# Kernel optimization log

Measured on AMD Instinct MI355X. Metric: run time of the kernel, lower is better.

Reference implementation:

```python
import jax, jax.numpy as jnp
import numpy as np

L, B, S, H = 4, 2, 2048, 1024
NH, HD, FFN = 16, 64, 4096
EPS = 1e-5


def setup_inputs() -> dict:
    key = jax.random.key(0)
    ks = jax.random.split(key, 6)
    std = 0.02
    return {
        "hidden_states": jax.random.normal(ks[0], (B, S, H), jnp.float32),
        "ln1_g": jnp.ones((L, H), jnp.float32),
        "ln1_b": jnp.zeros((L, H), jnp.float32),
        "Wqkv": jax.random.normal(ks[1], (L, H, 3 * H), jnp.float32) * std,
        "Wproj": jax.random.normal(ks[2], (L, H, H), jnp.float32) * std,
        "ln2_g": jnp.ones((L, H), jnp.float32),
        "ln2_b": jnp.zeros((L, H), jnp.float32),
        "Wfc1": jax.random.normal(ks[3], (L, H, FFN), jnp.float32) * std,
        "Wfc2": jax.random.normal(ks[4], (L, FFN, H), jnp.float32) * std,
        "lnf_g": jnp.ones((H,), jnp.float32),
        "lnf_b": jnp.zeros((H,), jnp.float32),
    }


def _layernorm(x, g, b):
    mu = jnp.mean(x, axis=-1, keepdims=True)
    var = jnp.mean(jnp.square(x - mu), axis=-1, keepdims=True)
    return (x - mu) * jax.lax.rsqrt(var + EPS) * g + b


def _block_forward(x, ln1_g, ln1_b, Wqkv, Wproj, ln2_g, ln2_b, Wfc1, Wfc2, lnf_g, lnf_b):
    scale = HD ** -0.5
    causal = jnp.tril(jnp.ones((S, S), bool))  # [S, S]

    def layer(x, p):
        g1, b1, wqkv, wproj, g2, b2, wfc1, wfc2 = p
        # Attention sub-block (pre-norm)
        h = _layernorm(x, g1, b1)
        qkv = (h @ wqkv).reshape(B, S, 3, NH, HD)
        q, k, v = qkv[:, :, 0], qkv[:, :, 1], qkv[:, :, 2]  # [B,S,NH,HD]
        scores = jnp.einsum("bqhd,bkhd->bhqk", q, k) * scale
        scores = jnp.where(causal, scores, -jnp.inf)
        probs = jax.nn.softmax(scores, axis=-1)
        attn = jnp.einsum("bhqk,bkhd->bqhd", probs, v).reshape(B, S, H)
        x = x + attn @ wproj
        # FFN sub-block (pre-norm)
        h = _layernorm(x, g2, b2)
        h = jax.nn.gelu(h @ wfc1, approximate=False) @ wfc2
        return x + h, None

    x, _ = jax.lax.scan(layer, x, (ln1_g, ln1_b, Wqkv, Wproj, ln2_g, ln2_b, Wfc1, Wfc2))
    return _layernorm(x, lnf_g, lnf_b)


def reference(hidden_states, ln1_g, ln1_b, Wqkv, Wproj, ln2_g, ln2_b, Wfc1, Wfc2, lnf_g, lnf_b):
    return _block_forward(hidden_states, ln1_g, ln1_b, Wqkv, Wproj, ln2_g, ln2_b, Wfc1, Wfc2, lnf_g, lnf_b)
```

## Files before the change

### kernel.cpp

```cpp
#include <hip/hip_runtime.h>
#include <hip/hip_bf16.h>
#include <math.h>

#define LYRS 4
#define BB   2
#define SS   2048
#define HH   1024
#define NHD  16
#define HDD  64
#define FFN_ 4096
#define BS   (BB*SS)
#define EPS_ 1e-5f

typedef __attribute__((ext_vector_type(8))) __bf16 bf16x8;
typedef __attribute__((ext_vector_type(4))) __bf16 bf16x4;
typedef __attribute__((ext_vector_type(4))) float f32x4;
typedef __attribute__((address_space(1))) void* gas_t;
typedef __attribute__((address_space(3))) void* las_t;

__device__ inline void async16(void* lds, const void* g) {
    __builtin_amdgcn_global_load_lds((gas_t)g, (las_t)lds, 16, 0, 0);
}

__device__ inline void storev(float* p, float v) { *p = v; }
__device__ inline void storev(__hip_bfloat16* p, float v) { *p = __float2bfloat16(v); }

template <typename OutT>
__global__ void ln_k(const float* __restrict__ x, const float* __restrict__ g,
                     const float* __restrict__ b, OutT* __restrict__ y) {
    const int row = blockIdx.x;
    const int tid = threadIdx.x;
    const float* xr = x + (size_t)row * HH;

    float v[4];
    float s = 0.f, s2 = 0.f;
#pragma unroll
    for (int i = 0; i < 4; ++i) {
        v[i] = xr[tid + i * 256];
        s  += v[i];
        s2 += v[i] * v[i];
    }
#pragma unroll
    for (int o = 1; o < 64; o <<= 1) {
        s  += __shfl_xor(s,  o);
        s2 += __shfl_xor(s2, o);
    }
    __shared__ float sh[8];
    const int wave = tid >> 6, lane = tid & 63;
    if (lane == 0) { sh[wave] = s; sh[4 + wave] = s2; }
    __syncthreads();
    if (tid == 0) {
        float ts  = sh[0] + sh[1] + sh[2] + sh[3];
        float ts2 = sh[4] + sh[5] + sh[6] + sh[7];
        float mu  = ts * (1.f / HH);
        sh[0] = mu;
        sh[1] = ts2 * (1.f / HH) - mu * mu;
    }
    __syncthreads();
    const float mu   = sh[0];
    const float rstd = rsqrtf(sh[1] + EPS_);
#pragma unroll
    for (int i = 0; i < 4; ++i) {
        int c = tid + i * 256;
        storev(&y[(size_t)row * HH + c], (v[i] - mu) * rstd * g[c] + b[c]);
    }
}

__global__ __launch_bounds__(256) void transpose_cast(const float* __restrict__ W,
                                                      __hip_bfloat16* __restrict__ WT,
                                                      int K, int N) {
    __shared__ float t[32][33];
    const int n0 = blockIdx.x * 32, k0 = blockIdx.y * 32;
    const int tx = threadIdx.x & 31, ty8 = threadIdx.x >> 5;
#pragma unroll
    for (int i = 0; i < 4; ++i) {
        int k = ty8 + i * 8;
        t[k][tx] = W[(size_t)(k0 + k) * N + n0 + tx];
    }
    __syncthreads();
#pragma unroll
    for (int i = 0; i < 4; ++i) {
        int n = ty8 + i * 8;
        WT[(size_t)(n0 + n) * K + k0 + tx] = __float2bfloat16(t[tx][n]);
    }
}

template <bool GELU, bool RES, int SPLITK, typename OutT>
__global__ __launch_bounds__(256) void gemm_bf16(
    const __hip_bfloat16* __restrict__ A,
    const __hip_bfloat16* __restrict__ BT,
    const float* __restrict__ R,
    OutT* __restrict__ C,
    int M, int N, int K)
{
    __shared__ unsigned short As[2][128 * 32];
    __shared__ unsigned short Bs[2][128 * 32];

    const int tid  = threadIdx.x;
    const int lane = tid & 63;
    const int wv   = tid >> 6;
    const int wy   = wv >> 1, wx = wv & 1;
    const int nby  = M >> 7;
    const int tiles = nby * (N >> 7);
    const int ks   = blockIdx.x / tiles;
    const int rem  = blockIdx.x % tiles;
    const int by   = rem % nby;
    const int bx   = rem / nby;
    const int row0 = by * 128;
    const int col0 = bx * 128;
    const int lm   = lane & 15;
    const int kq   = lane >> 4;

    const int Kslice = K / SPLITK;
    const int kbeg   = ks * Kslice;
    const int nsteps = Kslice >> 5;

    const unsigned short* Ag = (const unsigned short*)A;
    const unsigned short* Bg = (const unsigned short*)BT;

    const int li0 = tid, li1 = 256 + tid;
    const int r0 = li0 >> 2, c0 = (li0 & 3) << 3;
    const int r1 = li1 >> 2, c1 = (li1 & 3) << 3;
    const unsigned short* Ag0 = Ag + (size_t)(row0 + r0) * K + c0;
    const unsigned short* Ag1 = Ag + (size_t)(row0 + r1) * K + c1;
    const unsigned short* Bg0 = Bg + (size_t)(col0 + r0) * K + c0;
    const unsigned short* Bg1 = Bg + (size_t)(col0 + r1) * K + c1;

    auto stage = [&](int buf, int k) {
        async16(&As[buf][li0 * 8], Ag0 + k);
        async16(&As[buf][li1 * 8], Ag1 + k);
        async16(&Bs[buf][li0 * 8], Bg0 + k);
        async16(&Bs[buf][li1 * 8], Bg1 + k);
    };

    f32x4 acc[4][4] = {};

    stage(0, kbeg);
    __syncthreads();

    for (int s = 0; s < nsteps; ++s) {
        const int buf = s & 1;
        if (s + 1 < nsteps) stage(buf ^ 1, kbeg + ((s + 1) << 5));

        bf16x8 af[4], bfr[4];
#pragma unroll
        for (int i = 0; i < 4; ++i)
            af[i] = *(const bf16x8*)&As[buf][(wy * 64 + i * 16 + lm) * 32 + kq * 8];
#pragma unroll
        for (int j = 0; j < 4; ++j)
            bfr[j] = *(const bf16x8*)&Bs[buf][(wx * 64 + j * 16 + lm) * 32 + kq * 8];
#pragma unroll
        for (int i = 0; i < 4; ++i)
#pragma unroll
            for (int j = 0; j < 4; ++j)
                acc[i][j] = __builtin_amdgcn_mfma_f32_16x16x32_bf16(
                    af[i], bfr[j], acc[i][j], 0, 0, 0);

        __syncthreads();
    }

#pragma unroll
    for (int i = 0; i < 4; ++i) {
#pragma unroll
        for (int j = 0; j < 4; ++j) {
            int gc = col0 + wx * 64 + j * 16 + lm;
#pragma unroll
            for (int r = 0; r < 4; ++r) {
                int gr = row0 + wy * 64 + i * 16 + kq * 4 + r;
                float v = acc[i][j][r];
                if constexpr (SPLITK > 1) {
                    atomicAdd((float*)&C[(size_t)gr * N + gc], v);
                } else {
                    if (RES)  v += R[(size_t)gr * N + gc];
                    if (GELU) v = 0.5f * v * (1.0f + erff(v * 0.70710678118654752f));
                    storev(&C[(size_t)gr * N + gc], v);
                }
            }
        }
    }
}

__global__ __launch_bounds__(256) void attn_fa3(const __bf16* __restrict__ qkv,
                                                __bf16* __restrict__ out) {
    __shared__ __bf16 Ks[2][64 * 72];
    __shared__ __bf16 Vt[2][64 * 72];
    __shared__ __bf16 Ps[4][2][16 * 72];

    const int tid  = threadIdx.x;
    const int lane = tid & 63;
    const int w    = tid >> 6;
    const int lm   = lane & 15;
    const int kq   = lane >> 4;

    const int x  = blockIdx.x;
    const int bh = x & 31;
    const int h  = bh & 15;
    const int b  = bh >> 4;
    const int a  = (x >> 5) & 7;
    const int qt = (x & 256) ? (15 - a) : a;
    const int q0 = qt * 128;

    const size_t rs   = 3 * HH;
    const size_t base = (size_t)b * SS * rs + (size_t)h * HDD;

    const int krow0 = tid >> 3,        kc0 = (tid & 7) << 3;
    const int krow1 = (256 + tid) >> 3, kc1 = ((256 + tid) & 7) << 3;
    const int vkey  = tid & 63;
    const int vcb0  = (tid >> 6) << 3, vcb1 = ((256 + tid) >> 6) << 3;

    bf16x8 qf[2][2];
#pragma unroll
    for (int s = 0; s < 2; ++s)
#pragma unroll
        for (int kh = 0; kh < 2; ++kh) {
            bf16x8 t = *(const bf16x8*)&qkv[base +
                (size_t)(q0 + w * 32 + s * 16 + lm) * rs + kh * 32 + kq * 8];
#pragma unroll
            for (int j = 0; j < 8; ++j) t[j] = (__bf16)((float)t[j] * 0.125f);
            qf[s][kh] = t;
        }

    f32x4 ot[2][4] = {};
    float m_i[2] = {-INFINITY, -INFINITY};
    float l_i[2] = {0.f, 0.f};

    const int qmax_w = q0 + w * 32 + 31;
    const int ktmax  = (q0 + 127) >> 6;

    bf16x8 kr0, kr1, vr0, vr1;
    {
        const int k0 = 0;
        kr0 = *(const bf16x8*)&qkv[base + (size_t)(k0 + krow0) * rs + HH + kc0];
        kr1 = *(const bf16x8*)&qkv[base + (size_t)(k0 + krow1) * rs + HH + kc1];
        vr0 = *(const bf16x8*)&qkv[base + (size_t)(k0 + vkey) * rs + 2 * HH + vcb0];
        vr1 = *(const bf16x8*)&qkv[base + (size_t)(k0 + vkey) * rs + 2 * HH + vcb1];
        *(bf16x8*)&Ks[0][krow0 * 72 + kc0] = kr0;
        *(bf16x8*)&Ks[0][krow1 * 72 + kc1] = kr1;
#pragma unroll
        for (int j = 0; j < 8; ++j) Vt[0][(vcb0 + j) * 72 + vkey] = vr0[j];
#pragma unroll
        for (int j = 0; j < 8; ++j) Vt[0][(vcb1 + j) * 72 + vkey] = vr1[j];
    }
    __syncthreads();

    for (int kt = 0; kt <= ktmax; ++kt) {
        const int k0  = kt << 6;
        const int buf = kt & 1;

        if (kt < ktmax) {
            const int kn = k0 + 64;
            kr0 = *(const bf16x8*)&qkv[base + (size_t)(kn + krow0) * rs + HH + kc0];
            kr1 = *(const bf16x8*)&qkv[base + (size_t)(kn + krow1) * rs + HH + kc1];
            vr0 = *(const bf16x8*)&qkv[base + (size_t)(kn + vkey) * rs + 2 * HH + vcb0];
            vr1 = *(const bf16x8*)&qkv[base + (size_t)(kn + vkey) * rs + 2 * HH + vcb1];
        }

        if (k0 <= qmax_w) {
#pragma unroll
            for (int s = 0; s < 2; ++s) {
                f32x4 st[4] = {};
#pragma unroll
                for (int kh = 0; kh < 2; ++kh)
#pragma unroll
                    for (int m = 0; m < 4; ++m) {
                        bf16x8 kf = *(const bf16x8*)&Ks[buf][(m * 16 + lm) * 72 + kh * 32 + kq * 8];
                        st[m] = __builtin_amdgcn_mfma_f32_16x16x32_bf16(
                            kf, qf[s][kh], st[m], 0, 0, 0);
                    }

                const int qg = q0 + w * 32 + s * 16 + lm;
                if (k0 + 63 > q0 + w * 32 + s * 16) {
#pragma unroll
                    for (int m = 0; m < 4; ++m) {
                        int keyb = k0 + m * 16 + kq * 4;
#pragma unroll
                        for (int r = 0; r < 4; ++r)
                            if (keyb + r > qg) st[m][r] = -INFINITY;
                    }
                }

                float mloc = -INFINITY;
#pragma unroll
                for (int m = 0; m < 4; ++m)
#pragma unroll
                    for (int r = 0; r < 4; ++r) mloc = fmaxf(mloc, st[m][r]);
                mloc = fmaxf(mloc, __shfl_xor(mloc, 16));
                mloc = fmaxf(mloc, __shfl_xor(mloc, 32));
                float mn    = fmaxf(m_i[s], mloc);
                float alpha = __expf(m_i[s] - mn);
                m_i[s] = mn;

                float sum = 0.f;
#pragma unroll
                for (int m = 0; m < 4; ++m) {
                    bf16x4 pb;
#pragma unroll
                    for (int r = 0; r < 4; ++r) {
                        float p = __expf(st[m][r] - mn);
                        sum += p;
                        pb[r] = (__bf16)p;
                    }
                    *(bf16x4*)&Ps[w][s][lm * 72 + m * 16 + kq * 4] = pb;
                }
                sum += __shfl_xor(sum, 16);
                sum += __shfl_xor(sum, 32);
                l_i[s] = l_i[s] * alpha + sum;

#pragma unroll
                for (int dt = 0; dt < 4; ++dt) ot[s][dt] *= alpha;

#pragma unroll
                for (int kh = 0; kh < 2; ++kh) {
                    bf16x8 pf = *(const bf16x8*)&Ps[w][s][lm * 72 + kh * 32 + kq * 8];
#pragma unroll
                    for (int dt = 0; dt < 4; ++dt) {
                        bf16x8 vf = *(const bf16x8*)&Vt[buf][(dt * 16 + lm) * 72 + kh * 32 + kq * 8];
                        ot[s][dt] = __builtin_amdgcn_mfma_f32_16x16x32_bf16(
                            vf, pf, ot[s][dt], 0, 0, 0);
                    }
                }
            }
        }

        if (kt < ktmax) {
            const int nb = buf ^ 1;
            *(bf16x8*)&Ks[nb][krow0 * 72 + kc0] = kr0;
            *(bf16x8*)&Ks[nb][krow1 * 72 + kc1] = kr1;
#pragma unroll
            for (int j = 0; j < 8; ++j) Vt[nb][(vcb0 + j) * 72 + vkey] = vr0[j];
#pragma unroll
            for (int j = 0; j < 8; ++j) Vt[nb][(vcb1 + j) * 72 + vkey] = vr1[j];
            __syncthreads();
        }
    }

#pragma unroll
    for (int s = 0; s < 2; ++s) {
        float inv = 1.f / l_i[s];
        int qg = q0 + w * 32 + s * 16 + lm;
#pragma unroll
        for (int dt = 0; dt < 4; ++dt) {
            bf16x4 ob;
#pragma unroll
            for (int r = 0; r < 4; ++r) ob[r] = (__bf16)(ot[s][dt][r] * inv);
            *(bf16x4*)&out[(size_t)(b * SS + qg) * HH + h * HDD + dt * 16 + kq * 4] = ob;
        }
    }
}

extern "C" void kernel_launch(void* const* d_in, const int* in_sizes, int n_in,
                              void* d_out, int out_size, void* d_ws, size_t ws_size,
                              hipStream_t stream) {
    const float* hidden = (const float*)d_in[0];
    const float* ln1_g  = (const float*)d_in[1];
    const float* ln1_b  = (const float*)d_in[2];
    const float* Wqkv   = (const float*)d_in[3];
    const float* Wproj  = (const float*)d_in[4];
    const float* ln2_g  = (const float*)d_in[5];
    const float* ln2_b  = (const float*)d_in[6];
    const float* Wfc1   = (const float*)d_in[7];
    const float* Wfc2   = (const float*)d_in[8];
    const float* lnf_g  = (const float*)d_in[9];
    const float* lnf_b  = (const float*)d_in[10];

    float* x = (float*)d_out;

    char* p = (char*)d_ws;
    __hip_bfloat16* hbuf  = (__hip_bfloat16*)p; p += (size_t)BS * HH * 2;
    __hip_bfloat16* qkvb  = (__hip_bfloat16*)p; p += (size_t)BS * 3 * HH * 2;
    __hip_bfloat16* attnb = (__hip_bfloat16*)p; p += (size_t)BS * HH * 2;
    __hip_bfloat16* ffnb  = (__hip_bfloat16*)p; p += (size_t)BS * FFN_ * 2;
    __hip_bfloat16* wqkvT = (__hip_bfloat16*)p; p += (size_t)3 * HH * HH * 2;
    __hip_bfloat16* wprojT= (__hip_bfloat16*)p; p += (size_t)HH * HH * 2;
    __hip_bfloat16* wfc1T = (__hip_bfloat16*)p; p += (size_t)FFN_ * HH * 2;
    __hip_bfloat16* wfc2T = (__hip_bfloat16*)p; p += (size_t)HH * FFN_ * 2;

    hipMemcpyAsync(x, hidden, (size_t)BS * HH * sizeof(float),
                   hipMemcpyDeviceToDevice, stream);

    const int NBY = BS / 128;

    for (int lyr = 0; lyr < LYRS; ++lyr) {
        transpose_cast<<<dim3(3 * HH / 32, HH / 32), 256, 0, stream>>>(
            Wqkv + (size_t)lyr * HH * 3 * HH, wqkvT, HH, 3 * HH);
        transpose_cast<<<dim3(HH / 32, HH / 32), 256, 0, stream>>>(
            Wproj + (size_t)lyr * HH * HH, wprojT, HH, HH);
        transpose_cast<<<dim3(FFN_ / 32, HH / 32), 256, 0, stream>>>(
            Wfc1 + (size_t)lyr * HH * FFN_, wfc1T, HH, FFN_);
        transpose_cast<<<dim3(HH / 32, FFN_ / 32), 256, 0, stream>>>(
            Wfc2 + (size_t)lyr * FFN_ * HH, wfc2T, FFN_, HH);

        ln_k<__hip_bfloat16><<<BS, 256, 0, stream>>>(
            x, ln1_g + lyr * HH, ln1_b + lyr * HH, hbuf);
        gemm_bf16<false, false, 1, __hip_bfloat16>
            <<<(3 * HH / 128) * NBY, 256, 0, stream>>>(
            hbuf, wqkvT, nullptr, qkvb, BS, 3 * HH, HH);
        attn_fa3<<<512, 256, 0, stream>>>((const __bf16*)qkvb, (__bf16*)attnb);
        gemm_bf16<false, true, 1, float>
            <<<(HH / 128) * NBY, 256, 0, stream>>>(
            attnb, wprojT, x, x, BS, HH, HH);
        ln_k<__hip_bfloat16><<<BS, 256, 0, stream>>>(
            x, ln2_g + lyr * HH, ln2_b + lyr * HH, hbuf);
        gemm_bf16<true, false, 1, __hip_bfloat16>
            <<<(FFN_ / 128) * NBY, 256, 0, stream>>>(
            hbuf, wfc1T, nullptr, ffnb, BS, FFN_, HH);
        gemm_bf16<false, false, 2, float>
            <<<(HH / 128) * NBY * 2, 256, 0, stream>>>(
            ffnb, wfc2T, nullptr, x, BS, HH, FFN_);
    }
    ln_k<float><<<BS, 256, 0, stream>>>(x, lnf_g, lnf_b, x);
}
```

Measured before the change: 1.277 ms.

## Merge weight transposes, use wave-per-row layernorm, split-K proj, prioritize attention MFMA

Folds the four per-layer weight transpose launches into one launch that dispatches on block index. Layernorm now uses one wave per row with float4 loads and no LDS or block barriers. The attention projection switches to the split-K=2 GEMM variant, which presumably accumulates into x atomically, in place of the residual epilogue. s_setprio hints are wrapped around the MFMA sections of flash attention. Together these aim to cut launch count, barrier overhead and proj-GEMM under-occupancy, but split-K accumulation changes the order of the fp32 sums.

```diff
diff --git a/kernel.cpp b/kernel.cpp
--- a/kernel.cpp
+++ b/kernel.cpp
@@ -25,52 +25,65 @@
 __device__ inline void storev(float* p, float v) { *p = v; }
 __device__ inline void storev(__hip_bfloat16* p, float v) { *p = __float2bfloat16(v); }
 
+__device__ inline void store4(float* p, float a, float b, float c, float d) {
+    *(float4*)p = make_float4(a, b, c, d);
+}
+__device__ inline void store4(__hip_bfloat16* p, float a, float b, float c, float d) {
+    bf16x4 t; t[0] = (__bf16)a; t[1] = (__bf16)b; t[2] = (__bf16)c; t[3] = (__bf16)d;
+    *(bf16x4*)p = t;
+}
+
 template <typename OutT>
-__global__ void ln_k(const float* __restrict__ x, const float* __restrict__ g,
-                     const float* __restrict__ b, OutT* __restrict__ y) {
-    const int row = blockIdx.x;
-    const int tid = threadIdx.x;
-    const float* xr = x + (size_t)row * HH;
-
-    float v[4];
+__global__ __launch_bounds__(256) void ln_w(const float* __restrict__ x,
+                                            const float* __restrict__ g,
+                                            const float* __restrict__ b,
+                                            OutT* __restrict__ y) {
+    const int row  = blockIdx.x * 4 + (threadIdx.x >> 6);
+    const int lane = threadIdx.x & 63;
+    const float4* xr = (const float4*)(x + (size_t)row * HH);
+
+    float4 v[4];
     float s = 0.f, s2 = 0.f;
 #pragma unroll
     for (int i = 0; i < 4; ++i) {
-        v[i] = xr[tid + i * 256];
-        s  += v[i];
-        s2 += v[i] * v[i];
+        v[i] = xr[lane + i * 64];
+        s  += v[i].x + v[i].y + v[i].z + v[i].w;
+        s2 += v[i].x * v[i].x + v[i].y * v[i].y + v[i].z * v[i].z + v[i].w * v[i].w;
     }
 #pragma unroll
     for (int o = 1; o < 64; o <<= 1) {
         s  += __shfl_xor(s,  o);
         s2 += __shfl_xor(s2, o);
     }
-    __shared__ float sh[8];
-    const int wave = tid >> 6, lane = tid & 63;
-    if (lane == 0) { sh[wave] = s; sh[4 + wave] = s2; }
-    __syncthreads();
-    if (tid == 0) {
-        float ts  = sh[0] + sh[1] + sh[2] + sh[3];
-        float ts2 = sh[4] + sh[5] + sh[6] + sh[7];
-        float mu  = ts * (1.f / HH);
-        sh[0] = mu;
-        sh[1] = ts2 * (1.f / HH) - mu * mu;
-    }
-    __syncthreads();
-    const float mu   = sh[0];
-    const float rstd = rsqrtf(sh[1] + EPS_);
+    const float mu   = s * (1.f / HH);
+    const float rstd = rsqrtf(s2 * (1.f / HH) - mu * mu + EPS_);
 #pragma unroll
     for (int i = 0; i < 4; ++i) {
-        int c = tid + i * 256;
-        storev(&y[(size_t)row * HH + c], (v[i] - mu) * rstd * g[c] + b[c]);
-    }
-}
-
-__global__ __launch_bounds__(256) void transpose_cast(const float* __restrict__ W,
-                                                      __hip_bfloat16* __restrict__ WT,
-                                                      int K, int N) {
+        const int c = (lane + i * 64) * 4;
+        const float4 gv = *(const float4*)&g[c];
+        const float4 bv = *(const float4*)&b[c];
+        store4(&y[(size_t)row * HH + c],
+               (v[i].x - mu) * rstd * gv.x + bv.x,
+               (v[i].y - mu) * rstd * gv.y + bv.y,
+               (v[i].z - mu) * rstd * gv.z + bv.z,
+               (v[i].w - mu) * rstd * gv.w + bv.w);
+    }
+}
+
+__global__ __launch_bounds__(256) void transpose_all(
+    const float* __restrict__ Wqkv_l, const float* __restrict__ Wproj_l,
+    const float* __restrict__ Wfc1_l, const float* __restrict__ Wfc2_l,
+    __hip_bfloat16* __restrict__ wqkvT, __hip_bfloat16* __restrict__ wprojT,
+    __hip_bfloat16* __restrict__ wfc1T, __hip_bfloat16* __restrict__ wfc2T)
+{
     __shared__ float t[32][33];
-    const int n0 = blockIdx.x * 32, k0 = blockIdx.y * 32;
+    int tb = blockIdx.x;
+    const float* W; __hip_bfloat16* WT; int K, N, nx;
+    if (tb < 3072)      {            W = Wqkv_l;  WT = wqkvT;  K = HH;   N = 3 * HH; nx = 96;  }
+    else if (tb < 4096) { tb -= 3072; W = Wproj_l; WT = wprojT; K = HH;   N = HH;     nx = 32;  }
+    else if (tb < 8192) { tb -= 4096; W = Wfc1_l;  WT = wfc1T;  K = HH;   N = FFN_;   nx = 128; }
+    else                { tb -= 8192; W = Wfc2_l;  WT = wfc2T;  K = FFN_; N = HH;     nx = 32;  }
+    const int n0 = (tb % nx) * 32, k0 = (tb / nx) * 32;
     const int tx = threadIdx.x & 31, ty8 = threadIdx.x >> 5;
 #pragma unroll
     for (int i = 0; i < 4; ++i) {
@@ -259,6 +272,7 @@
 #pragma unroll
             for (int s = 0; s < 2; ++s) {
                 f32x4 st[4] = {};
+                __builtin_amdgcn_s_setprio(1);
 #pragma unroll
                 for (int kh = 0; kh < 2; ++kh)
 #pragma unroll
@@ -267,6 +281,7 @@
                         st[m] = __builtin_amdgcn_mfma_f32_16x16x32_bf16(
                             kf, qf[s][kh], st[m], 0, 0, 0);
                     }
+                __builtin_amdgcn_s_setprio(0);
 
                 const int qg = q0 + w * 32 + s * 16 + lm;
                 if (k0 + 63 > q0 + w * 32 + s * 16) {
@@ -309,6 +324,7 @@
 #pragma unroll
                 for (int dt = 0; dt < 4; ++dt) ot[s][dt] *= alpha;
 
+                __builtin_amdgcn_s_setprio(1);
 #pragma unroll
                 for (int kh = 0; kh < 2; ++kh) {
                     bf16x8 pf = *(const bf16x8*)&Ps[w][s][lm * 72 + kh * 32 + kq * 8];
@@ -319,6 +335,7 @@
                             vf, pf, ot[s][dt], 0, 0, 0);
                     }
                 }
+                __builtin_amdgcn_s_setprio(0);
             }
         }
 
@@ -381,25 +398,23 @@
     const int NBY = BS / 128;
 
     for (int lyr = 0; lyr < LYRS; ++lyr) {
-        transpose_cast<<<dim3(3 * HH / 32, HH / 32), 256, 0, stream>>>(
-            Wqkv + (size_t)lyr * HH * 3 * HH, wqkvT, HH, 3 * HH);
-        transpose_cast<<<dim3(HH / 32, HH / 32), 256, 0, stream>>>(
-            Wproj + (size_t)lyr * HH * HH, wprojT, HH, HH);
-        transpose_cast<<<dim3(FFN_ / 32, HH / 32), 256, 0, stream>>>(
-            Wfc1 + (size_t)lyr * HH * FFN_, wfc1T, HH, FFN_);
-        transpose_cast<<<dim3(HH / 32, FFN_ / 32), 256, 0, stream>>>(
-            Wfc2 + (size_t)lyr * FFN_ * HH, wfc2T, FFN_, HH);
-
-        ln_k<__hip_bfloat16><<<BS, 256, 0, stream>>>(
+        transpose_all<<<12288, 256, 0, stream>>>(
+            Wqkv  + (size_t)lyr * HH * 3 * HH,
+            Wproj + (size_t)lyr * HH * HH,
+            Wfc1  + (size_t)lyr * HH * FFN_,
+            Wfc2  + (size_t)lyr * FFN_ * HH,
+            wqkvT, wprojT, wfc1T, wfc2T);
+
+        ln_w<__hip_bfloat16><<<BS / 4, 256, 0, stream>>>(
             x, ln1_g + lyr * HH, ln1_b + lyr * HH, hbuf);
         gemm_bf16<false, false, 1, __hip_bfloat16>
             <<<(3 * HH / 128) * NBY, 256, 0, stream>>>(
             hbuf, wqkvT, nullptr, qkvb, BS, 3 * HH, HH);
         attn_fa3<<<512, 256, 0, stream>>>((const __bf16*)qkvb, (__bf16*)attnb);
-        gemm_bf16<false, true, 1, float>
-            <<<(HH / 128) * NBY, 256, 0, stream>>>(
-            attnb, wprojT, x, x, BS, HH, HH);
-        ln_k<__hip_bfloat16><<<BS, 256, 0, stream>>>(
+        gemm_bf16<false, false, 2, float>
+            <<<(HH / 128) * NBY * 2, 256, 0, stream>>>(
+            attnb, wprojT, nullptr, x, BS, HH, HH);
+        ln_w<__hip_bfloat16><<<BS / 4, 256, 0, stream>>>(
             x, ln2_g + lyr * HH, ln2_b + lyr * HH, hbuf);
         gemm_bf16<true, false, 1, __hip_bfloat16>
             <<<(FFN_ / 128) * NBY, 256, 0, stream>>>(
@@ -408,5 +423,5 @@
             <<<(HH / 128) * NBY * 2, 256, 0, stream>>>(
             ffnb, wfc2T, nullptr, x, BS, HH, FFN_);
     }
-    ln_k<float><<<BS, 256, 0, stream>>>(x, lnf_g, lnf_b, x);
-}
+    ln_w<float><<<BS / 4, 256, 0, stream>>>(x, lnf_g, lnf_b, x);
+}
```

Result: slower. 1.317 ms (+3.1%).
